# Performance work log

Hardware: AMD Instinct MI355X
Metric: run time of the kernel (lower is better)

## Reference

```python
import jax, jax.numpy as jnp
import numpy as np

B, T, V, E, U = 64, 512, 32000, 300, 1024


def setup_inputs() -> dict:
    key = jax.random.key(0)
    k0, k1, k2, k3 = jax.random.split(key, 4)
    x = jax.random.randint(k0, (B, T), 0, V)
    hidden = jnp.zeros((B, U), jnp.float32)
    embedding_matrix = jax.random.normal(k1, (V, E), jnp.float32) * 0.1
    kernel = jax.random.normal(k2, (E, 3 * U), jnp.float32) * (1.0 / np.sqrt(E))
    recurrent_kernel = jax.random.normal(k3, (U, 3 * U), jnp.float32) * (1.0 / np.sqrt(U))
    bias = jnp.zeros((2, 3 * U), jnp.float32)
    return {"x": x, "hidden": hidden, "embedding_matrix": embedding_matrix,
            "kernel": kernel, "recurrent_kernel": recurrent_kernel, "bias": bias}


def _gru(x_tokens, h0, emb, kernel, rec_kernel, bias):
    u = h0.shape[-1]
    xe = emb[x_tokens]                                  # [B,T,E] embedding lookup
    # Precompute input projection for all timesteps (Keras reset_after=True):
    xp = jnp.einsum('bte,eg->btg', xe, kernel) + bias[0]  # [B,T,3U]
    xz = jnp.swapaxes(xp[..., :u], 0, 1)                # [T,B,U]
    xr = jnp.swapaxes(xp[..., u:2 * u], 0, 1)
    xh = jnp.swapaxes(xp[..., 2 * u:], 0, 1)
    rb = bias[1]

    def step(h, xs):
        xz_t, xr_t, xh_t = xs
        inner = h @ rec_kernel + rb                     # [B,3U]
        rz, rr, rh = inner[:, :u], inner[:, u:2 * u], inner[:, 2 * u:]
        z = jax.nn.sigmoid(xz_t + rz)
        r = jax.nn.sigmoid(xr_t + rr)
        hh = jnp.tanh(xh_t + r * rh)
        h_new = z * h + (1.0 - z) * hh
        return h_new, h_new

    state, outs = jax.lax.scan(step, h0, (xz, xr, xh))
    return jnp.swapaxes(outs, 0, 1), state              # [B,T,U], [B,U]


def reference(x, hidden, embedding_matrix, kernel, recurrent_kernel, bias):
    return _gru(x, hidden, embedding_matrix, kernel, recurrent_kernel, bias)
```

## Files before the change

kernel.cpp:

```cpp
#include <hip/hip_runtime.h>

typedef _Float16 f16;
typedef _Float16 half8 __attribute__((ext_vector_type(8)));
typedef float f32x4 __attribute__((ext_vector_type(4)));
typedef unsigned long long u64;

#define B_  64
#define T_  512
#define V_  32000
#define E_  300
#define EP  320
#define U_  1024
#define G3  3072

#define OFF_XE   0ull
#define OFF_HX   OFF_XE
#define OFF_CTR2 (OFF_XE + 2ull*B_*U_*2)
#define OFF_W1T  (OFF_XE  + (size_t)B_*T_*EP*2)
#define OFF_W2F  (OFF_W1T + (size_t)G3*EP*2)
#define OFF_XP   (OFF_W2F + (size_t)U_*G3*2)

__device__ __forceinline__ void barrier_lds() {
    asm volatile("s_waitcnt lgkmcnt(0)\n\ts_barrier" ::: "memory");
}

#define WLOAD(dst, src) \
    asm volatile("global_load_dwordx4 %0, %1, off" : "=v"(dst) : "v"(src) : "memory")
#define CLOAD(dst, src) \
    asm volatile("global_load_dwordx4 %0, %1, off sc0 sc1" : "=v"(dst) : "v"(src) : "memory")
#define VMFENCE() do {                                      \
    asm volatile("s_waitcnt vmcnt(0)" ::: "memory");        \
    __builtin_amdgcn_sched_barrier(0);                      \
} while (0)


__global__ void k_gather(const int* __restrict__ x, const float* __restrict__ emb,
                         f16* __restrict__ xe) {
    int row  = blockIdx.x * 4 + (threadIdx.x >> 6);
    int lane = threadIdx.x & 63;
    int tok  = x[row];
    const float* er = emb + (size_t)tok * E_;
    f16* xr = xe + (size_t)row * EP;
#pragma unroll
    for (int e = lane; e < EP; e += 64) {
        float v = (e < E_) ? er[e] : 0.f;
        xr[e] = (f16)v;
    }
}

__global__ void k_w1t(const float* __restrict__ w1, f16* __restrict__ w1t) {
    int n = blockIdx.x;
    int k = threadIdx.x;
    float v = (k < E_) ? w1[(size_t)k * G3 + n] : 0.f;
    w1t[(size_t)n * EP + k] = (f16)v;
}

__global__ void k_w2f(const float* __restrict__ w2, f16* __restrict__ w2f) {
    int g    = blockIdx.x * 256 + threadIdx.x;
    int lane = g & 63;
    int kt   = (g >> 6) & 31;
    int nt   = g >> 11;
    int krow = kt * 32 + (lane >> 4) * 8;
    int n    = nt * 16 + (lane & 15);
    f16* dst = w2f + ((size_t)(nt * 32 + kt) * 64 + lane) * 8;
#pragma unroll
    for (int j = 0; j < 8; ++j)
        dst[j] = (f16)w2[(size_t)(krow + j) * G3 + n];
}

__global__ void k_hinit(const float* __restrict__ h0, f16* __restrict__ hx) {
    int i = blockIdx.x * 256 + threadIdx.x;
    f16 a = (f16)h0[2 * i], b = (f16)h0[2 * i + 1];
    unsigned lo = *(unsigned short*)&a, hi = *(unsigned short*)&b;
    __hip_atomic_store((unsigned*)hx + i, lo | (hi << 16),
                       __ATOMIC_RELAXED, __HIP_MEMORY_SCOPE_AGENT);
}

__global__ __launch_bounds__(256) void k_xp(const f16* __restrict__ xe,
                                            const f16* __restrict__ w1t,
                                            const float* __restrict__ bias0,
                                            f16* __restrict__ xp) {
    __shared__ __align__(16) f16 As[128 * 32];
    __shared__ __align__(16) f16 Bs[128 * 32];
    const int tid  = threadIdx.x;
    const int lane = tid & 63;
    const int w    = tid >> 6;
    const int wm   = w >> 1, wn = w & 1;
    const int n0   = blockIdx.x * 128;
    const int m0   = blockIdx.y * 128;

    f32x4 acc[4][4];
    const f32x4 z4 = {0.f, 0.f, 0.f, 0.f};
#pragma unroll
    for (int i = 0; i < 4; ++i)
#pragma unroll
        for (int j = 0; j < 4; ++j) acc[i][j] = z4;

    for (int kk = 0; kk < EP / 32; ++kk) {
        int k0 = kk * 32;
        __syncthreads();
#pragma unroll
        for (int c = 0; c < 2; ++c) {
            int t2 = tid + 256 * c;
            int row = t2 >> 2, kq = t2 & 3;
            ((half8*)As)[t2] = *(const half8*)(xe  + (size_t)(m0 + row) * EP + k0 + kq * 8);
            ((half8*)Bs)[t2] = *(const half8*)(w1t + (size_t)(n0 + row) * EP + k0 + kq * 8);
        }
        __syncthreads();
        half8 a[4], b[4];
#pragma unroll
        for (int i = 0; i < 4; ++i) {
            a[i] = ((half8*)As)[(wm * 64 + i * 16 + (lane & 15)) * 4 + (lane >> 4)];
            b[i] = ((half8*)Bs)[(wn * 64 + i * 16 + (lane & 15)) * 4 + (lane >> 4)];
        }
#pragma unroll
        for (int i = 0; i < 4; ++i)
#pragma unroll
            for (int j = 0; j < 4; ++j)
                acc[i][j] = __builtin_amdgcn_mfma_f32_16x16x32_f16(a[i], b[j], acc[i][j], 0, 0, 0);
    }

    float bv[4];
#pragma unroll
    for (int j = 0; j < 4; ++j) bv[j] = bias0[n0 + wn * 64 + j * 16 + (lane & 15)];
#pragma unroll
    for (int i = 0; i < 4; ++i)
#pragma unroll
        for (int j = 0; j < 4; ++j)
#pragma unroll
            for (int e = 0; e < 4; ++e) {
                int rl  = wm * 64 + i * 16 + (lane >> 4) * 4 + e;
                int bt  = m0 + rl;
                int tt  = bt & (T_ - 1);
                int bb  = bt >> 9;
                int col = n0 + wn * 64 + j * 16 + (lane & 15);
                xp[((size_t)tt * B_ + bb) * G3 + col] = (f16)(acc[i][j][e] + bv[j]);
            }
}

__global__ __launch_bounds__(512, 2) void k_rec(const f16* __restrict__ xp,
                                                const f16* __restrict__ w2f,
                                                const float* __restrict__ bias1,
                                                const float* __restrict__ h0,
                                                f16* __restrict__ hx,
                                                float* __restrict__ out,
                                                unsigned* __restrict__ ctr) {
    const int tid  = threadIdx.x;
    const int lane = tid & 63;
    const int wave = tid >> 6;
    const int uw   = wave >> 2;
    const int kw   = wave & 3;
    const int rw   = blockIdx.x & 3;
    const int ut2  = blockIdx.x >> 2;
    const int ut16 = ut2 * 2 + uw;

    __shared__ __align__(16) f16   hs[16 * 1024];
    __shared__ __align__(16) float red[8][3][64][5];

    half8 bw[3][8];
#pragma unroll
    for (int g = 0; g < 3; ++g) {
        int nt = g * 64 + ut16;
#pragma unroll
        for (int k8 = 0; k8 < 8; ++k8) {
            int kt = kw * 8 + k8;
            const f16* src = w2f + ((size_t)(nt * 32 + kt) * 64 + lane) * 8;
            WLOAD(bw[g][k8], src);
        }
    }
    VMFENCE();

    const int row  = tid >> 5;
    const int u32  = tid & 31;
    const int rowg = rw * 16 + row;
    const int ug   = ut2 * 32 + u32;
    float h = h0[rowg * U_ + ug];
    const float bz = bias1[ug], br = bias1[U_ + ug], bh = bias1[2 * U_ + ug];
    const int lsrc = (row >> 2) * 16 + (u32 & 15);
    const int ei   = row & 3;
    const int uwq  = u32 >> 4;
    const f32x4 z4 = {0.f, 0.f, 0.f, 0.f};
    unsigned* myflags = ctr + rw * 2048;

    const f16* gsb = hx + (size_t)rowg * U_ + (size_t)u32 * 8;
    half8* ldsdst  = (half8*)(hs + row * 1024) + (u32 ^ (row & 7));
    const int rrow = lane & 15;
    const int rsw  = rrow & 7;
    const f16* hrow = hs + rrow * 1024 + kw * 256;
    const int rq   = lane >> 4;
    float* outrow = out + (size_t)rowg * T_ * U_ + ug;

    const f16* xpb = xp + (size_t)rowg * G3 + ug;
    float xz = (float)xpb[0], xr = (float)xpb[(size_t)U_], xh = (float)xpb[(size_t)2 * U_];

#pragma unroll 1
    for (int t = 0; t < T_; ++t) {
        const f16* gs = gsb + (size_t)(t & 1) * (B_ * U_);
        half8 v0, v1, v2, v3;
        CLOAD(v0, gs);
        CLOAD(v1, gs + 256);
        CLOAD(v2, gs + 512);
        CLOAD(v3, gs + 768);
        asm volatile("s_waitcnt vmcnt(0)" ::: "memory");
        ldsdst[0]  = v0;
        ldsdst[32] = v1;
        ldsdst[64] = v2;
        ldsdst[96] = v3;
        if (t) outrow[(size_t)(t - 1) * U_] = h;
        barrier_lds();

        half8 af[8];
#pragma unroll
        for (int k8 = 0; k8 < 8; ++k8)
            af[k8] = *(const half8*)(hrow + (((rq + 4 * k8) ^ rsw) << 3));

        int tn = (t < T_ - 1) ? t + 1 : t;
        const f16* xpn = xp + ((size_t)tn * B_ + rowg) * G3 + ug;
        float xzn = (float)xpn[0], xrn = (float)xpn[(size_t)U_], xhn = (float)xpn[(size_t)2 * U_];

        f32x4 acc[3] = {z4, z4, z4};
#pragma unroll
        for (int k8 = 0; k8 < 8; ++k8)
#pragma unroll
            for (int g = 0; g < 3; ++g)
                acc[g] = __builtin_amdgcn_mfma_f32_16x16x32_f16(af[k8], bw[g][k8], acc[g], 0, 0, 0);

#pragma unroll
        for (int g = 0; g < 3; ++g)
#pragma unroll
            for (int e = 0; e < 4; ++e)
                red[wave][g][lane][e] = acc[g][e];
        barrier_lds();

        float sz = 0.f, sr = 0.f, sh = 0.f;
#pragma unroll
        for (int k2 = 0; k2 < 4; ++k2) {
            int w2 = uwq * 4 + k2;
            sz += red[w2][0][lsrc][ei];
            sr += red[w2][1][lsrc][ei];
            sh += red[w2][2][lsrc][ei];
        }

        float zg = 1.f / (1.f + expf(-(xz + sz + bz)));
        float rg = 1.f / (1.f + expf(-(xr + sr + br)));
        float hh = tanhf(xh + rg * (sh + bh));
        h = zg * h + (1.f - zg) * hh;

        f16 hf = (f16)h;
        unsigned my = *(unsigned short*)&hf;
        unsigned nb = __shfl_down(my, 1);
        if ((u32 & 1) == 0) {
            unsigned* dst = (unsigned*)(hx + (size_t)((t + 1) & 1) * (B_ * U_)
                                        + (size_t)rowg * U_ + ug);
            __hip_atomic_store(dst, my | (nb << 16),
                               __ATOMIC_RELAXED, __HIP_MEMORY_SCOPE_AGENT);
        }

        __syncthreads();
        if (wave == 0) {
            if (lane == 0)
                __hip_atomic_store(myflags + ut2 * 32, (unsigned)(t + 1),
                                   __ATOMIC_RELAXED, __HIP_MEMORY_SCOPE_AGENT);
            const unsigned* pf = myflags + (lane & 31) * 32;
            unsigned v;
            do {
                v = __hip_atomic_load(pf, __ATOMIC_RELAXED, __HIP_MEMORY_SCOPE_AGENT);
            } while (__ballot(v < (unsigned)(t + 1)) != 0ull);
        }
        __syncthreads();

        xz = xzn; xr = xrn; xh = xhn;
    }
    outrow[(size_t)(T_ - 1) * U_] = h;
    out[(size_t)B_ * T_ * U_ + (size_t)rowg * U_ + ug] = h;
}

extern "C" void kernel_launch(void* const* d_in, const int* in_sizes, int n_in,
                              void* d_out, int out_size, void* d_ws, size_t ws_size,
                              hipStream_t stream) {
    const int*   x    = (const int*)d_in[0];
    const float* h0   = (const float*)d_in[1];
    const float* emb  = (const float*)d_in[2];
    const float* w1   = (const float*)d_in[3];
    const float* w2   = (const float*)d_in[4];
    const float* bias = (const float*)d_in[5];
    float* out = (float*)d_out;
    char*  ws  = (char*)d_ws;

    f16*      xe   = (f16*)(ws + OFF_XE);
    f16*      w1t  = (f16*)(ws + OFF_W1T);
    f16*      w2f  = (f16*)(ws + OFF_W2F);
    f16*      xp   = (f16*)(ws + OFF_XP);
    f16*      hx   = (f16*)(ws + OFF_HX);
    unsigned* ctr  = (unsigned*)(ws + OFF_CTR2);

    k_gather<<<B_ * T_ / 4, 256, 0, stream>>>(x, emb, xe);
    k_w1t<<<G3, EP, 0, stream>>>(w1, w1t);
    k_w2f<<<(192 * 32 * 64) / 256, 256, 0, stream>>>(w2, w2f);
    k_xp<<<dim3(G3 / 128, B_ * T_ / 128), 256, 0, stream>>>(xe, w1t, bias, xp);

    hipMemsetAsync(ctr, 0, 4 * 2048 * sizeof(unsigned), stream);
    k_hinit<<<(B_ * U_ / 2) / 256, 256, 0, stream>>>(h0, hx);

    const f16*   xp_c   = xp;
    const f16*   w2f_c  = w2f;
    const float* bias1  = bias + G3;
    void* args[] = {(void*)&xp_c, (void*)&w2f_c, (void*)&bias1, (void*)&h0,
                    (void*)&hx, (void*)&out, (void*)&ctr};
    if (hipLaunchCooperativeKernel((const void*)k_rec, dim3(128), dim3(512),
                                   args, 0, stream) != hipSuccess) {
        k_rec<<<128, 512, 0, stream>>>(xp_c, w2f_c, bias1, h0, hx, out, ctr);
    }
}
```

Baseline: 1.595 ms.

## Replace flag-counter barrier with parity-tagged hidden state and triple buffering

Removes the per-step flag store/poll and the two block-wide syncs. Instead, the low mantissa bit of each fp16 hidden value carries a step-parity tag, and consumers spin on the data loads themselves until every element shows the expected parity. A third hidden buffer lets a fast block write step t+1 without overwriting data a slow block still reads. This cuts one global round trip per timestep, at the cost of one bit of fp16 precision in h and repeated reload loops while waiting.

Measured after the change: 1.389 ms. 1.15x faster.

```diff
diff --git a/kernel.cpp b/kernel.cpp
--- a/kernel.cpp
+++ b/kernel.cpp
@@ -3,6 +3,7 @@
 typedef _Float16 f16;
 typedef _Float16 half8 __attribute__((ext_vector_type(8)));
 typedef float f32x4 __attribute__((ext_vector_type(4)));
+typedef unsigned u32x4 __attribute__((ext_vector_type(4)));
 typedef unsigned long long u64;
 
 #define B_  64
@@ -12,10 +13,11 @@
 #define EP  320
 #define U_  1024
 #define G3  3072
+#define BU  (B_ * U_)
+#define BUB (B_ * U_ * 2)
 
 #define OFF_XE   0ull
 #define OFF_HX   OFF_XE
-#define OFF_CTR2 (OFF_XE + 2ull*B_*U_*2)
 #define OFF_W1T  (OFF_XE  + (size_t)B_*T_*EP*2)
 #define OFF_W2F  (OFF_W1T + (size_t)G3*EP*2)
 #define OFF_XP   (OFF_W2F + (size_t)U_*G3*2)
@@ -71,7 +73,7 @@
 __global__ void k_hinit(const float* __restrict__ h0, f16* __restrict__ hx) {
     int i = blockIdx.x * 256 + threadIdx.x;
     f16 a = (f16)h0[2 * i], b = (f16)h0[2 * i + 1];
-    unsigned lo = *(unsigned short*)&a, hi = *(unsigned short*)&b;
+    unsigned lo = (*(unsigned short*)&a) | 1u, hi = (*(unsigned short*)&b) | 1u;
     __hip_atomic_store((unsigned*)hx + i, lo | (hi << 16),
                        __ATOMIC_RELAXED, __HIP_MEMORY_SCOPE_AGENT);
 }
@@ -143,8 +145,7 @@
                                                 const float* __restrict__ bias1,
                                                 const float* __restrict__ h0,
                                                 f16* __restrict__ hx,
-                                                float* __restrict__ out,
-                                                unsigned* __restrict__ ctr) {
+                                                float* __restrict__ out) {
     const int tid  = threadIdx.x;
     const int lane = tid & 63;
     const int wave = tid >> 6;
@@ -180,7 +181,6 @@
     const int ei   = row & 3;
     const int uwq  = u32 >> 4;
     const f32x4 z4 = {0.f, 0.f, 0.f, 0.f};
-    unsigned* myflags = ctr + rw * 2048;
 
     const f16* gsb = hx + (size_t)rowg * U_ + (size_t)u32 * 8;
     half8* ldsdst  = (half8*)(hs + row * 1024) + (u32 ^ (row & 7));
@@ -193,20 +193,33 @@
     const f16* xpb = xp + (size_t)rowg * G3 + ug;
     float xz = (float)xpb[0], xr = (float)xpb[(size_t)U_], xh = (float)xpb[(size_t)2 * U_];
 
+    int rb = 0, wb = 1;
+
 #pragma unroll 1
     for (int t = 0; t < T_; ++t) {
-        const f16* gs = gsb + (size_t)(t & 1) * (B_ * U_);
-        half8 v0, v1, v2, v3;
-        CLOAD(v0, gs);
-        CLOAD(v1, gs + 256);
-        CLOAD(v2, gs + 512);
-        CLOAD(v3, gs + 768);
-        asm volatile("s_waitcnt vmcnt(0)" ::: "memory");
-        ldsdst[0]  = v0;
-        ldsdst[32] = v1;
-        ldsdst[64] = v2;
-        ldsdst[96] = v3;
         if (t) outrow[(size_t)(t - 1) * U_] = h;
+
+        const unsigned pm = (unsigned)((t + 1) & 1) * 0x00010001u;
+        const f16* gs = gsb + (size_t)rb * BU;
+        u32x4 a0, a1, a2, a3;
+        bool ok0 = false, ok1 = false, ok2 = false, ok3 = false;
+        while (true) {
+            if (!ok0) CLOAD(a0, gs);
+            if (!ok1) CLOAD(a1, gs + 256);
+            if (!ok2) CLOAD(a2, gs + 512);
+            if (!ok3) CLOAD(a3, gs + 768);
+            VMFENCE();
+            const unsigned m = 0x00010001u;
+            if (!ok0) ok0 = ((((a0[0]^pm)|(a0[1]^pm)|(a0[2]^pm)|(a0[3]^pm)) & m) == 0u);
+            if (!ok1) ok1 = ((((a1[0]^pm)|(a1[1]^pm)|(a1[2]^pm)|(a1[3]^pm)) & m) == 0u);
+            if (!ok2) ok2 = ((((a2[0]^pm)|(a2[1]^pm)|(a2[2]^pm)|(a2[3]^pm)) & m) == 0u);
+            if (!ok3) ok3 = ((((a3[0]^pm)|(a3[1]^pm)|(a3[2]^pm)|(a3[3]^pm)) & m) == 0u);
+            if (__ballot(!(ok0 & ok1 & ok2 & ok3)) == 0ull) break;
+        }
+        ((u32x4*)ldsdst)[0]  = a0;
+        ((u32x4*)ldsdst)[32] = a1;
+        ((u32x4*)ldsdst)[64] = a2;
+        ((u32x4*)ldsdst)[96] = a3;
         barrier_lds();
 
         half8 af[8];
@@ -247,28 +260,16 @@
         h = zg * h + (1.f - zg) * hh;
 
         f16 hf = (f16)h;
-        unsigned my = *(unsigned short*)&hf;
+        unsigned my = ((unsigned)*(unsigned short*)&hf & 0xFFFEu) | (unsigned)(t & 1);
         unsigned nb = __shfl_down(my, 1);
         if ((u32 & 1) == 0) {
-            unsigned* dst = (unsigned*)(hx + (size_t)((t + 1) & 1) * (B_ * U_)
+            unsigned* dst = (unsigned*)(hx + (size_t)wb * BU
                                         + (size_t)rowg * U_ + ug);
             __hip_atomic_store(dst, my | (nb << 16),
                                __ATOMIC_RELAXED, __HIP_MEMORY_SCOPE_AGENT);
         }
 
-        __syncthreads();
-        if (wave == 0) {
-            if (lane == 0)
-                __hip_atomic_store(myflags + ut2 * 32, (unsigned)(t + 1),
-                                   __ATOMIC_RELAXED, __HIP_MEMORY_SCOPE_AGENT);
-            const unsigned* pf = myflags + (lane & 31) * 32;
-            unsigned v;
-            do {
-                v = __hip_atomic_load(pf, __ATOMIC_RELAXED, __HIP_MEMORY_SCOPE_AGENT);
-            } while (__ballot(v < (unsigned)(t + 1)) != 0ull);
-        }
-        __syncthreads();
-
+        rb = wb; wb = (wb + 1 == 3) ? 0 : wb + 1;
         xz = xzn; xr = xrn; xh = xhn;
     }
     outrow[(size_t)(T_ - 1) * U_] = h;
@@ -292,23 +293,23 @@
     f16*      w2f  = (f16*)(ws + OFF_W2F);
     f16*      xp   = (f16*)(ws + OFF_XP);
     f16*      hx   = (f16*)(ws + OFF_HX);
-    unsigned* ctr  = (unsigned*)(ws + OFF_CTR2);
 
     k_gather<<<B_ * T_ / 4, 256, 0, stream>>>(x, emb, xe);
     k_w1t<<<G3, EP, 0, stream>>>(w1, w1t);
     k_w2f<<<(192 * 32 * 64) / 256, 256, 0, stream>>>(w2, w2f);
     k_xp<<<dim3(G3 / 128, B_ * T_ / 128), 256, 0, stream>>>(xe, w1t, bias, xp);
 
-    hipMemsetAsync(ctr, 0, 4 * 2048 * sizeof(unsigned), stream);
+    hipMemsetAsync(ws + OFF_HX + 1ull * BUB, 0xFF, BUB, stream);
+    hipMemsetAsync(ws + OFF_HX + 2ull * BUB, 0x00, BUB, stream);
     k_hinit<<<(B_ * U_ / 2) / 256, 256, 0, stream>>>(h0, hx);
 
     const f16*   xp_c   = xp;
     const f16*   w2f_c  = w2f;
     const float* bias1  = bias + G3;
     void* args[] = {(void*)&xp_c, (void*)&w2f_c, (void*)&bias1, (void*)&h0,
-                    (void*)&hx, (void*)&out, (void*)&ctr};
+                    (void*)&hx, (void*)&out};
     if (hipLaunchCooperativeKernel((const void*)k_rec, dim3(128), dim3(512),
                                    args, 0, stream) != hipSuccess) {
-        k_rec<<<128, 512, 0, stream>>>(xp_c, w2f_c, bias1, h0, hx, out, ctr);
-    }
-}
+        k_rec<<<128, 512, 0, stream>>>(xp_c, w2f_c, bias1, h0, hx, out);
+    }
+}
```
